# Optimization experiments

Measured on AMD Instinct MI355X. Metric: run time of the kernel, lower is better.

The kernel has to match this reference:

```python
import jax, jax.numpy as jnp
import numpy as np

DIM = 1024
NUM_HEADS = 16
HEAD_DIM = DIM // NUM_HEADS


def setup_inputs() -> dict:
    key = jax.random.key(0)
    k_x, k_wqkv, k_bqkv, k_wo, k_bo = jax.random.split(key, 5)
    B, N = 2, 2048
    s = 1.0 / np.sqrt(DIM)
    return {
        "x": jax.random.normal(k_x, (B, N, DIM), dtype=jnp.float32),
        "w_qkv": jax.random.uniform(k_wqkv, (DIM, 3 * DIM), jnp.float32, -s, s),
        "b_qkv": jax.random.uniform(k_bqkv, (3 * DIM,), jnp.float32, -s, s),
        "w_out": jax.random.uniform(k_wo, (DIM, DIM), jnp.float32, -s, s),
        "b_out": jax.random.uniform(k_bo, (DIM,), jnp.float32, -s, s),
    }


def reference(x, w_qkv, b_qkv, w_out, b_out):
    B, N, D = x.shape
    H, Hd = NUM_HEADS, HEAD_DIM
    scale = Hd ** -0.5
    qkv = x @ w_qkv + b_qkv                      # [B,N,3D]
    qkv = qkv.reshape(B, N, 3, H, Hd).transpose(2, 0, 3, 1, 4)  # [3,B,H,N,Hd]
    q, k, v = qkv[0], qkv[1], qkv[2]
    scores = jnp.einsum("bhqd,bhkd->bhqk", q, k) * scale
    attn = jax.nn.softmax(scores, axis=-1)
    out = jnp.einsum("bhqk,bhkd->bhqd", attn, v)  # [B,H,N,Hd]
    out = out.transpose(0, 2, 1, 3).reshape(B, N, D)
    return out @ w_out + b_out
```

## Files before the change

kernel.cpp:

```cpp
#include <hip/hip_runtime.h>
#include <stdint.h>

#define D_MODEL 1024
#define NHEADS 16
#define HDIM 64
#define BATCH 2
#define SEQ 2048
#define MTOK (BATCH*SEQ)

typedef unsigned short u16;
typedef __attribute__((ext_vector_type(8))) __bf16 bf16x8;
typedef __attribute__((ext_vector_type(8))) unsigned short u16x8;
typedef __attribute__((ext_vector_type(4))) unsigned short u16x4;
typedef __attribute__((ext_vector_type(4))) float f32x4;

__device__ __forceinline__ u16 f2bf(float f) {
  union { float f; uint32_t u; } v; v.f = f;
  uint32_t u = v.u;
  u += 0x7fffu + ((u >> 16) & 1u);
  return (u16)(u >> 16);
}

__device__ __forceinline__ u16 f2bf_hw(float f) {
  return __builtin_bit_cast(u16, (__bf16)f);
}

__device__ __forceinline__ void async16(u16* lds, const u16* g) {
  __builtin_amdgcn_global_load_lds(
      (__attribute__((address_space(1))) void*)(u16*)g,
      (__attribute__((address_space(3))) void*)lds,
      16, 0, 0);
}

__device__ __forceinline__ void transpose_cast_body(
    const float* __restrict__ in, u16* __restrict__ out, int R, int C,
    int bid, int tid, float (*tile)[33])
{
  int nCB = C >> 5;
  int bc = bid % nCB, br = bid / nCB;
  int r0 = br * 32, c0 = bc * 32;
  int tx = tid & 31, ty = tid >> 5;
#pragma unroll
  for (int i = 0; i < 4; ++i)
    tile[ty + i*8][tx] = in[(size_t)(r0 + ty + i*8) * C + c0 + tx];
  __syncthreads();
#pragma unroll
  for (int i = 0; i < 4; ++i)
    out[(size_t)(c0 + ty + i*8) * R + r0 + tx] = f2bf(tile[tx][ty + i*8]);
}

__global__ __launch_bounds__(256) void prep_kernel(
    const float* __restrict__ x, const float* __restrict__ w_qkv,
    const float* __restrict__ w_out,
    u16* __restrict__ x_bf, u16* __restrict__ wqkv_t, u16* __restrict__ wout_t)
{
  __shared__ float tile[32][33];
  int bid = blockIdx.x, tid = threadIdx.x;
  if (bid < 2048) {
    int i = bid * 256 + tid;
    const float4* p = (const float4*)(x + (size_t)i * 8);
    float4 a = p[0], b = p[1];
    u16x8 r;
    r[0]=f2bf(a.x); r[1]=f2bf(a.y); r[2]=f2bf(a.z); r[3]=f2bf(a.w);
    r[4]=f2bf(b.x); r[5]=f2bf(b.y); r[6]=f2bf(b.z); r[7]=f2bf(b.w);
    *(u16x8*)(x_bf + (size_t)i * 8) = r;
  } else if (bid < 2048 + 3072) {
    transpose_cast_body(w_qkv, wqkv_t, 1024, 3072, bid - 2048, tid, tile);
  } else {
    transpose_cast_body(w_out, wout_t, 1024, 1024, bid - 5120, tid, tile);
  }
}

template <int EPI>
__global__ __launch_bounds__(512, 4) void gemm_bt_kernel(
    const u16* __restrict__ A, const u16* __restrict__ Bt,
    const float* __restrict__ bias,
    float* __restrict__ outF,
    u16* __restrict__ qb, u16* __restrict__ kb, u16* __restrict__ vt,
    int M, int Nn, int K)
{
  __shared__ alignas(16) u16 As[2][128 * 64];
  __shared__ alignas(16) u16 Bs[2][128 * 64];

  const int tid = threadIdx.x;
  const int wid = tid >> 6, lane = tid & 63;
  const int col = lane & 15, kg = lane >> 4;
  const int csw = (col & 7) << 3;

  const int nTN = Nn >> 7;
  int bidx = blockIdx.x;
  {
    int cpx = gridDim.x >> 3;
    bidx = (bidx & 7) * cpx + (bidx >> 3);
  }
  const int tile_m = (bidx / nTN) << 7;
  const int tile_n = (bidx % nTN) << 7;
  const int wm = (wid >> 2) << 6;
  const int wn = (wid & 3) << 5;

  f32x4 acc[4][2] = {};

  const int sr = tid >> 3;
  const int sc = (tid & 7) << 3;
  const int ssc = sc ^ ((sr & 7) << 3);

#define STAGE(buf, kt)                                                        \
  {                                                                           \
    _Pragma("unroll")                                                         \
    for (int i = 0; i < 2; ++i)                                               \
      async16(&As[buf][(i*64 + sr) * 64 + sc],                                \
              A + (size_t)(tile_m + i*64 + sr) * K + (kt)*64 + ssc);          \
    _Pragma("unroll")                                                         \
    for (int i = 0; i < 2; ++i)                                               \
      async16(&Bs[buf][(i*64 + sr) * 64 + sc],                                \
              Bt + (size_t)(tile_n + i*64 + sr) * K + (kt)*64 + ssc);         \
  }

  const int nk = K >> 6;
  STAGE(0, 0);
  __syncthreads();
  int cur = 0;

  for (int kt = 0; kt < nk; ++kt) {
    if (kt + 1 < nk) STAGE(cur ^ 1, kt + 1);

#pragma unroll
    for (int ks = 0; ks < 2; ++ks) {
      bf16x8 af[4], bfv[2];
#pragma unroll
      for (int i = 0; i < 4; ++i)
        af[i] = *(const bf16x8*)&As[cur][(wm + i*16 + col) * 64 + ((ks*32 + kg*8) ^ csw)];
#pragma unroll
      for (int j = 0; j < 2; ++j)
        bfv[j] = *(const bf16x8*)&Bs[cur][(wn + j*16 + col) * 64 + ((ks*32 + kg*8) ^ csw)];
#pragma unroll
      for (int i = 0; i < 4; ++i)
#pragma unroll
        for (int j = 0; j < 2; ++j)
          acc[i][j] = __builtin_amdgcn_mfma_f32_16x16x32_bf16(af[i], bfv[j], acc[i][j], 0, 0, 0);
    }

    __syncthreads();
    cur ^= 1;
  }
#undef STAGE

#pragma unroll
  for (int i = 0; i < 4; ++i) {
#pragma unroll
    for (int jn = 0; jn < 2; ++jn) {
      const int gcol = tile_n + wn + jn*16 + col;
      const float bv = bias[gcol];
      const int grow0 = tile_m + wm + i*16 + kg*4;
      if (EPI == 1) {
#pragma unroll
        for (int j = 0; j < 4; ++j)
          outF[(size_t)(grow0 + j) * Nn + gcol] = acc[i][jn][j] + bv;
      } else {
        const int btok = grow0 >> 11, tok0 = grow0 & 2047;
        const int which = gcol >> 10, f = gcol & 1023;
        const int h = f >> 6, hd = f & 63;
        if (which == 2) {
          u16x4 pk;
#pragma unroll
          for (int j = 0; j < 4; ++j) pk[j] = f2bf(acc[i][jn][j] + bv);
          *(u16x4*)&vt[((size_t)(btok*NHEADS + h) * HDIM + hd) * SEQ + tok0] = pk;
        } else {
#pragma unroll
          for (int j = 0; j < 4; ++j) {
            float val = acc[i][jn][j] + bv;
            size_t dst = ((size_t)(btok*NHEADS + h) * SEQ + tok0 + j) * HDIM + hd;
            if (which == 0) qb[dst] = f2bf(val * 0.18033688f);
            else            kb[dst] = f2bf(val);
          }
        }
      }
    }
  }
}

__global__ __launch_bounds__(256, 2) void attn_kernel(
    const u16* __restrict__ qb, const u16* __restrict__ kb,
    const u16* __restrict__ vt, u16* __restrict__ ao)
{
  __shared__ alignas(16) u16 Ks[128 * 64];
  __shared__ alignas(16) u16 Vs[64 * 128];
  __shared__ alignas(16) u16 Pl[4][32 * 128];

  const int tid = threadIdx.x, wid = tid >> 6, lane = tid & 63;
  const int col = lane & 15, kg = lane >> 4;
  const int csw = (col & 7) << 3;

  int bidx = blockIdx.x;
  bidx = (bidx & 7) * 64 + (bidx >> 3);
  const int bh = bidx >> 4;
  const int qt = bidx & 15;

  const u16* Qh = qb + (size_t)bh * SEQ * HDIM;
  const u16* Kh = kb + (size_t)bh * SEQ * HDIM;
  const u16* Vh = vt + (size_t)bh * SEQ * HDIM;

  const int q0 = qt * 128 + wid * 32;
  bf16x8 qf[2][2];
#pragma unroll
  for (int mf = 0; mf < 2; ++mf)
#pragma unroll
    for (int ks = 0; ks < 2; ++ks)
      qf[mf][ks] = *(const bf16x8*)(Qh + (size_t)(q0 + mf*16 + col) * HDIM + ks*32 + kg*8);

  float l_run[2] = {0.f, 0.f};
  f32x4 o[2][4] = {};

  u16* Pw = Pl[wid];

  const int krow = tid >> 1, kc = (tid & 1) << 5, ksw = (krow & 7) << 3;
  const int vrow = tid >> 2, vc = (tid & 3) << 5, vsw = (vrow & 7) << 3;

  u16x8 kreg[4], vreg[4];
#define LOAD_TILES(t)                                                               \
  {                                                                                 \
    _Pragma("unroll")                                                               \
    for (int i = 0; i < 4; ++i)                                                     \
      kreg[i] = *(const u16x8*)(Kh + (size_t)((t)*128 + krow) * HDIM + kc + i*8);   \
    _Pragma("unroll")                                                               \
    for (int i = 0; i < 4; ++i)                                                     \
      vreg[i] = *(const u16x8*)(Vh + (size_t)vrow * SEQ + (t)*128 + vc + i*8);      \
  }

  LOAD_TILES(0);

  for (int t = 0; t < 16; ++t) {
    __syncthreads();
#pragma unroll
    for (int i = 0; i < 4; ++i)
      *(u16x8*)&Ks[krow * 64 + ((kc + i*8) ^ ksw)] = kreg[i];
#pragma unroll
    for (int i = 0; i < 4; ++i)
      *(u16x8*)&Vs[vrow * 128 + ((vc + i*8) ^ vsw)] = vreg[i];
    __syncthreads();
    if (t < 15) LOAD_TILES(t + 1);

    f32x4 s[2][8] = {};
#pragma unroll
    for (int ks = 0; ks < 2; ++ks) {
#pragma unroll
      for (int nf = 0; nf < 8; ++nf) {
        bf16x8 kf = *(const bf16x8*)&Ks[(nf*16 + col) * 64 + ((ks*32 + kg*8) ^ csw)];
        s[0][nf] = __builtin_amdgcn_mfma_f32_16x16x32_bf16(kf, qf[0][ks], s[0][nf], 0, 0, 0);
        s[1][nf] = __builtin_amdgcn_mfma_f32_16x16x32_bf16(kf, qf[1][ks], s[1][nf], 0, 0, 0);
      }
    }

#pragma unroll
    for (int mf = 0; mf < 2; ++mf) {
      f32x4 sum4 = {0.f, 0.f, 0.f, 0.f};
#pragma unroll
      for (int nf = 0; nf < 8; ++nf) {
#pragma unroll
        for (int r = 0; r < 4; ++r)
          s[mf][nf][r] = __builtin_amdgcn_exp2f(s[mf][nf][r]);
        sum4[0] += s[mf][nf][0]; sum4[1] += s[mf][nf][1];
        sum4[2] += s[mf][nf][2]; sum4[3] += s[mf][nf][3];
      }
      l_run[mf] += (sum4[0] + sum4[1]) + (sum4[2] + sum4[3]);
#pragma unroll
      for (int nf = 0; nf < 8; ++nf) {
        u16x4 pk;
        pk[0] = f2bf_hw(s[mf][nf][0]); pk[1] = f2bf_hw(s[mf][nf][1]);
        pk[2] = f2bf_hw(s[mf][nf][2]); pk[3] = f2bf_hw(s[mf][nf][3]);
        *(u16x4*)&Pw[(mf*16 + col) * 128 + ((nf*16 + kg*4) ^ csw)] = pk;
      }
    }

#pragma unroll
    for (int ks = 0; ks < 4; ++ks) {
      bf16x8 pf0 = *(const bf16x8*)&Pw[(col) * 128 + ((ks*32 + kg*8) ^ csw)];
      bf16x8 pf1 = *(const bf16x8*)&Pw[(16 + col) * 128 + ((ks*32 + kg*8) ^ csw)];
#pragma unroll
      for (int hf = 0; hf < 4; ++hf) {
        bf16x8 vf = *(const bf16x8*)&Vs[(hf*16 + col) * 128 + ((ks*32 + kg*8) ^ csw)];
        o[0][hf] = __builtin_amdgcn_mfma_f32_16x16x32_bf16(vf, pf0, o[0][hf], 0, 0, 0);
        o[1][hf] = __builtin_amdgcn_mfma_f32_16x16x32_bf16(vf, pf1, o[1][hf], 0, 0, 0);
      }
    }
  }

  const int bb = bh >> 4, h = bh & 15;
#pragma unroll
  for (int mf = 0; mf < 2; ++mf) {
    float l = l_run[mf];
    l += __shfl_xor(l, 16);
    l += __shfl_xor(l, 32);
    float inv = 1.0f / l;
    int nrow = q0 + mf*16 + col;
#pragma unroll
    for (int hf = 0; hf < 4; ++hf) {
      u16x4 pk;
#pragma unroll
      for (int j = 0; j < 4; ++j) pk[j] = f2bf(o[mf][hf][j] * inv);
      int feat = h*64 + hf*16 + kg*4;
      *(u16x4*)&ao[(size_t)(bb * SEQ + nrow) * D_MODEL + feat] = pk;
    }
  }
#undef LOAD_TILES
}

extern "C" void kernel_launch(void* const* d_in, const int* in_sizes, int n_in,
                              void* d_out, int out_size, void* d_ws, size_t ws_size,
                              hipStream_t stream)
{
  const float* x     = (const float*)d_in[0];
  const float* w_qkv = (const float*)d_in[1];
  const float* b_qkv = (const float*)d_in[2];
  const float* w_out = (const float*)d_in[3];
  const float* b_out = (const float*)d_in[4];
  float* out = (float*)d_out;
  (void)in_sizes; (void)n_in; (void)out_size; (void)ws_size;

  char* ws = (char*)d_ws;
  u16* x_bf   = (u16*)(ws);
  u16* wqkv_t = (u16*)(ws + (size_t)( 8 << 20));
  u16* wout_t = (u16*)(ws + (size_t)(14 << 20));
  u16* qb     = (u16*)(ws + (size_t)(16 << 20));
  u16* kb     = (u16*)(ws + (size_t)(24 << 20));
  u16* vt     = (u16*)(ws + (size_t)(32 << 20));
  u16* ao     = (u16*)(ws + (size_t)(40 << 20));

  prep_kernel<<<2048 + 3072 + 1024, 256, 0, stream>>>(x, w_qkv, w_out, x_bf, wqkv_t, wout_t);

  gemm_bt_kernel<0><<<(MTOK/128)*(3072/128), 512, 0, stream>>>(
      x_bf, wqkv_t, b_qkv, nullptr, qb, kb, vt, MTOK, 3072, 1024);

  attn_kernel<<<32*16, 256, 0, stream>>>(qb, kb, vt, ao);

  gemm_bt_kernel<1><<<(MTOK/128)*(1024/128), 512, 0, stream>>>(
      ao, wout_t, b_out, out, nullptr, nullptr, nullptr, MTOK, 1024, 1024);
}
```

Before: 116.8 us.

## Switch attention to 32x32x16 MFMA and keep P in registers via permlane swap

The attention kernel now uses 32x32x16 bf16 MFMAs instead of 16x16x32, so each wave computes its 32 query rows against 128 keys as four 32x32 score tiles. The softmax probabilities are packed with v_cvt_pk_bf16_f32 and rearranged into the B-operand layout with v_permlane32_swap. This removes the per-wave LDS staging buffer for P and its write/read round trip, and cuts LDS use, which may allow more occupancy. In exchange it relies on gfx950-specific permlane instructions and puts a larger 16-float accumulator per tile in registers.

```diff
diff --git a/kernel.cpp b/kernel.cpp
--- a/kernel.cpp
+++ b/kernel.cpp
@@ -13,6 +13,8 @@
 typedef __attribute__((ext_vector_type(8))) unsigned short u16x8;
 typedef __attribute__((ext_vector_type(4))) unsigned short u16x4;
 typedef __attribute__((ext_vector_type(4))) float f32x4;
+typedef __attribute__((ext_vector_type(16))) float f32x16;
+typedef __attribute__((ext_vector_type(2))) unsigned int u32x2;
 
 __device__ __forceinline__ u16 f2bf(float f) {
   union { float f; uint32_t u; } v; v.f = f;
@@ -23,6 +25,21 @@
 
 __device__ __forceinline__ u16 f2bf_hw(float f) {
   return __builtin_bit_cast(u16, (__bf16)f);
+}
+
+__device__ __forceinline__ unsigned cvtpk(float a, float b) {
+  unsigned r;
+  asm("v_cvt_pk_bf16_f32 %0, %1, %2" : "=v"(r) : "v"(a), "v"(b));
+  return r;
+}
+
+__device__ __forceinline__ u32x2 plswap(unsigned a, unsigned b) {
+#if __has_builtin(__builtin_amdgcn_permlane32_swap)
+  return __builtin_amdgcn_permlane32_swap(a, b, false, false);
+#else
+  asm("v_permlane32_swap_b32 %0, %1" : "+v"(a), "+v"(b));
+  u32x2 r; r.x = a; r.y = b; return r;
+#endif
 }
 
 __device__ __forceinline__ void async16(u16* lds, const u16* g) {
@@ -185,11 +202,10 @@
 {
   __shared__ alignas(16) u16 Ks[128 * 64];
   __shared__ alignas(16) u16 Vs[64 * 128];
-  __shared__ alignas(16) u16 Pl[4][32 * 128];
 
   const int tid = threadIdx.x, wid = tid >> 6, lane = tid & 63;
-  const int col = lane & 15, kg = lane >> 4;
-  const int csw = (col & 7) << 3;
+  const int c31 = lane & 31, hi = lane >> 5;
+  const int rsw = (lane & 7) << 3;
 
   int bidx = blockIdx.x;
   bidx = (bidx & 7) * 64 + (bidx >> 3);
@@ -201,17 +217,13 @@
   const u16* Vh = vt + (size_t)bh * SEQ * HDIM;
 
   const int q0 = qt * 128 + wid * 32;
-  bf16x8 qf[2][2];
-#pragma unroll
-  for (int mf = 0; mf < 2; ++mf)
-#pragma unroll
-    for (int ks = 0; ks < 2; ++ks)
-      qf[mf][ks] = *(const bf16x8*)(Qh + (size_t)(q0 + mf*16 + col) * HDIM + ks*32 + kg*8);
-
-  float l_run[2] = {0.f, 0.f};
-  f32x4 o[2][4] = {};
-
-  u16* Pw = Pl[wid];
+  bf16x8 qf[4];
+#pragma unroll
+  for (int kk = 0; kk < 4; ++kk)
+    qf[kk] = *(const bf16x8*)(Qh + (size_t)(q0 + c31) * HDIM + kk*16 + hi*8);
+
+  float l_run = 0.f;
+  f32x16 o[2] = {};
 
   const int krow = tid >> 1, kc = (tid & 1) << 5, ksw = (krow & 7) << 3;
   const int vrow = tid >> 2, vc = (tid & 3) << 5, vsw = (vrow & 7) << 3;
@@ -240,66 +252,61 @@
     __syncthreads();
     if (t < 15) LOAD_TILES(t + 1);
 
-    f32x4 s[2][8] = {};
-#pragma unroll
-    for (int ks = 0; ks < 2; ++ks) {
-#pragma unroll
-      for (int nf = 0; nf < 8; ++nf) {
-        bf16x8 kf = *(const bf16x8*)&Ks[(nf*16 + col) * 64 + ((ks*32 + kg*8) ^ csw)];
-        s[0][nf] = __builtin_amdgcn_mfma_f32_16x16x32_bf16(kf, qf[0][ks], s[0][nf], 0, 0, 0);
-        s[1][nf] = __builtin_amdgcn_mfma_f32_16x16x32_bf16(kf, qf[1][ks], s[1][nf], 0, 0, 0);
-      }
-    }
-
-#pragma unroll
-    for (int mf = 0; mf < 2; ++mf) {
-      f32x4 sum4 = {0.f, 0.f, 0.f, 0.f};
-#pragma unroll
-      for (int nf = 0; nf < 8; ++nf) {
-#pragma unroll
-        for (int r = 0; r < 4; ++r)
-          s[mf][nf][r] = __builtin_amdgcn_exp2f(s[mf][nf][r]);
-        sum4[0] += s[mf][nf][0]; sum4[1] += s[mf][nf][1];
-        sum4[2] += s[mf][nf][2]; sum4[3] += s[mf][nf][3];
-      }
-      l_run[mf] += (sum4[0] + sum4[1]) + (sum4[2] + sum4[3]);
-#pragma unroll
-      for (int nf = 0; nf < 8; ++nf) {
+    f32x16 s[4] = {};
+#pragma unroll
+    for (int kk = 0; kk < 4; ++kk) {
+#pragma unroll
+      for (int nt = 0; nt < 4; ++nt) {
+        bf16x8 kf = *(const bf16x8*)&Ks[(nt*32 + c31) * 64 + ((kk*16 + hi*8) ^ rsw)];
+        s[nt] = __builtin_amdgcn_mfma_f32_32x32x16_bf16(kf, qf[kk], s[nt], 0, 0, 0);
+      }
+    }
+
+#pragma unroll
+    for (int nt = 0; nt < 4; ++nt) {
+      float sum = 0.f;
+#pragma unroll
+      for (int r = 0; r < 16; ++r) {
+        s[nt][r] = __builtin_amdgcn_exp2f(s[nt][r]);
+        sum += s[nt][r];
+      }
+      l_run += sum;
+    }
+
+#pragma unroll
+    for (int kk = 0; kk < 8; ++kk) {
+      const int nt = kk >> 1, rb = (kk & 1) * 8;
+      unsigned A0 = cvtpk(s[nt][rb+0], s[nt][rb+1]);
+      unsigned A1 = cvtpk(s[nt][rb+2], s[nt][rb+3]);
+      unsigned B0 = cvtpk(s[nt][rb+4], s[nt][rb+5]);
+      unsigned B1 = cvtpk(s[nt][rb+6], s[nt][rb+7]);
+      u32x2 p0 = plswap(A0, B0);
+      u32x2 p1 = plswap(A1, B1);
+      union { unsigned w[4]; bf16x8 v; } pf;
+      pf.w[0] = p0.x; pf.w[1] = p1.x; pf.w[2] = p0.y; pf.w[3] = p1.y;
+#pragma unroll
+      for (int dt = 0; dt < 2; ++dt) {
+        bf16x8 vf = *(const bf16x8*)&Vs[(dt*32 + c31) * 128 + ((kk*16 + hi*8) ^ rsw)];
+        o[dt] = __builtin_amdgcn_mfma_f32_32x32x16_bf16(vf, pf.v, o[dt], 0, 0, 0);
+      }
+    }
+  }
+
+  const int bb = bh >> 4, h = bh & 15;
+  {
+    float l = l_run + __shfl_xor(l_run, 32);
+    float inv = 1.0f / l;
+    const int nrow = q0 + c31;
+#pragma unroll
+    for (int dt = 0; dt < 2; ++dt) {
+#pragma unroll
+      for (int tq = 0; tq < 4; ++tq) {
         u16x4 pk;
-        pk[0] = f2bf_hw(s[mf][nf][0]); pk[1] = f2bf_hw(s[mf][nf][1]);
-        pk[2] = f2bf_hw(s[mf][nf][2]); pk[3] = f2bf_hw(s[mf][nf][3]);
-        *(u16x4*)&Pw[(mf*16 + col) * 128 + ((nf*16 + kg*4) ^ csw)] = pk;
-      }
-    }
-
-#pragma unroll
-    for (int ks = 0; ks < 4; ++ks) {
-      bf16x8 pf0 = *(const bf16x8*)&Pw[(col) * 128 + ((ks*32 + kg*8) ^ csw)];
-      bf16x8 pf1 = *(const bf16x8*)&Pw[(16 + col) * 128 + ((ks*32 + kg*8) ^ csw)];
-#pragma unroll
-      for (int hf = 0; hf < 4; ++hf) {
-        bf16x8 vf = *(const bf16x8*)&Vs[(hf*16 + col) * 128 + ((ks*32 + kg*8) ^ csw)];
-        o[0][hf] = __builtin_amdgcn_mfma_f32_16x16x32_bf16(vf, pf0, o[0][hf], 0, 0, 0);
-        o[1][hf] = __builtin_amdgcn_mfma_f32_16x16x32_bf16(vf, pf1, o[1][hf], 0, 0, 0);
-      }
-    }
-  }
-
-  const int bb = bh >> 4, h = bh & 15;
-#pragma unroll
-  for (int mf = 0; mf < 2; ++mf) {
-    float l = l_run[mf];
-    l += __shfl_xor(l, 16);
-    l += __shfl_xor(l, 32);
-    float inv = 1.0f / l;
-    int nrow = q0 + mf*16 + col;
-#pragma unroll
-    for (int hf = 0; hf < 4; ++hf) {
-      u16x4 pk;
-#pragma unroll
-      for (int j = 0; j < 4; ++j) pk[j] = f2bf(o[mf][hf][j] * inv);
-      int feat = h*64 + hf*16 + kg*4;
-      *(u16x4*)&ao[(size_t)(bb * SEQ + nrow) * D_MODEL + feat] = pk;
+#pragma unroll
+        for (int j = 0; j < 4; ++j) pk[j] = f2bf(o[dt][tq*4 + j] * inv);
+        int feat = h*64 + dt*32 + tq*8 + hi*4;
+        *(u16x4*)&ao[(size_t)(bb * SEQ + nrow) * D_MODEL + feat] = pk;
+      }
     }
   }
 #undef LOAD_TILES
```

After: 112.8 us. 3.4% less time.
